# Performance work log

Hardware: AMD Instinct MI355X
Metric: run time of the kernel (lower is better)

Reference implementation:

```python
import jax, jax.numpy as jnp
import numpy as np

N_NODES = 50000
N_EDGES = 800000
IN_CH = 128
OUT_CH = 64


def setup_inputs() -> dict:
    key = jax.random.key(0)
    ks = jax.random.split(key, 8)
    cat = IN_CH + OUT_CH
    scale = 1.0 / np.sqrt(cat)
    return {
        "x": jax.random.normal(ks[0], (N_NODES, IN_CH), dtype=jnp.float32),
        "edge_index": jax.random.randint(ks[1], (2, N_EDGES), 0, N_NODES, dtype=jnp.int64),
        "edge_weight": jax.random.uniform(ks[2], (N_EDGES,), dtype=jnp.float32),
        "hidden_state": jax.random.normal(ks[3], (N_NODES, OUT_CH), dtype=jnp.float32),
        "W_z": jax.random.normal(ks[4], (cat, OUT_CH), dtype=jnp.float32) * scale,
        "b_z": jnp.zeros((OUT_CH,), dtype=jnp.float32),
        "W_r": jax.random.normal(ks[5], (cat, OUT_CH), dtype=jnp.float32) * scale,
        "b_r": jnp.zeros((OUT_CH,), dtype=jnp.float32),
        "W_h": jax.random.normal(ks[6], (cat, OUT_CH), dtype=jnp.float32) * scale,
        "b_h": jnp.zeros((OUT_CH,), dtype=jnp.float32),
    }


def _gcn_norm(row, col, w, num_nodes):
    # PyG GCNConv normalization with self-loops (fill_value=1):
    # norm_e = deg[row]^-1/2 * w_e * deg[col]^-1/2 over loop-augmented edges
    loops = jnp.arange(num_nodes, dtype=row.dtype)
    row = jnp.concatenate([row, loops])
    col = jnp.concatenate([col, loops])
    w = jnp.concatenate([w, jnp.ones((num_nodes,), dtype=w.dtype)])
    deg = jax.ops.segment_sum(w, col, num_segments=num_nodes)
    dinv = jnp.where(deg > 0, jax.lax.rsqrt(deg), 0.0)
    norm = dinv[row] * w * dinv[col]
    return row, col, norm


def _gcn_conv(x_cat, W, b, row, col, norm, num_nodes):
    h = x_cat @ W                                   # (N, out)
    msg = h[row] * norm[:, None]                    # (E+N, out) gather + scale
    out = jax.ops.segment_sum(msg, col, num_segments=num_nodes)
    return out + b


def reference(x, edge_index, edge_weight, hidden_state,
              W_z, b_z, W_r, b_r, W_h, b_h):
    n = x.shape[0]
    row, col, norm = _gcn_norm(edge_index[0], edge_index[1], edge_weight, n)
    xh = jnp.concatenate([x, hidden_state], axis=1)
    z = jax.nn.sigmoid(_gcn_conv(xh, W_z, b_z, row, col, norm, n))
    r = jax.nn.sigmoid(_gcn_conv(xh, W_r, b_r, row, col, norm, n))
    xrh = jnp.concatenate([x, r * hidden_state], axis=1)
    h_cand = jnp.tanh(_gcn_conv(xrh, W_h, b_h, row, col, norm, n))
    return z * hidden_state + (1.0 - z) * h_cand
```

## Files before the change

kernel.cpp:

```cpp
#include <hip/hip_runtime.h>
#include <hip/hip_bf16.h>
#include <cstdint>
#include <cstddef>

#define IN_CH   128
#define OUT_CH  64
#define CAT_CH  192

typedef short bf16x8 __attribute__((ext_vector_type(8)));
typedef float f32x4  __attribute__((ext_vector_type(4)));
typedef float f32x2  __attribute__((ext_vector_type(2)));
typedef unsigned long long u64;
typedef unsigned int u32;

__device__ __forceinline__ float sigmoidf_(float x) { return 1.f / (1.f + __expf(-x)); }

__device__ __forceinline__ unsigned short f2bf(float f) {
    u32 u = __float_as_uint(f);
    u32 r = (u + 0x7fffu + ((u >> 16) & 1u)) >> 16;
    return (unsigned short)r;
}
__device__ __forceinline__ u32 pk2bf(float a, float b) {
    return (u32)f2bf(a) | ((u32)f2bf(b) << 16);
}
__device__ __forceinline__ float bflo(u32 v) { return __uint_as_float(v << 16); }
__device__ __forceinline__ float bfhi(u32 v) { return __uint_as_float(v & 0xffff0000u); }

__device__ __forceinline__ unsigned char f2e4m3(float f) {
    u32 p = __builtin_amdgcn_cvt_pk_fp8_f32(f, f, 0, false);
    return (unsigned char)p;
}
template <bool HI>
__device__ __forceinline__ f32x2 fp8pk(u32 v) {
    return __builtin_amdgcn_cvt_pk_f32_fp8((int)v, HI);
}

__device__ __forceinline__ int load_col(const void* ei, int i, int E, int f) {
    return f ? ((const int*)ei)[E + i] : (int)((const long long*)ei)[E + i];
}
__device__ __forceinline__ int load_row(const void* ei, int i, int E, int f) {
    return f ? ((const int*)ei)[i] : (int)((const long long*)ei)[i];
}

__global__ void prep_kernel(int4* __restrict__ zdst, int n16,
                            const unsigned int* __restrict__ ei, int* __restrict__ flag,
                            const float* __restrict__ Wz, const float* __restrict__ Wr,
                            const float* __restrict__ Wh,
                            unsigned short* __restrict__ Bzrt, unsigned short* __restrict__ Wht,
                            int gZ) {
    int b = blockIdx.x, t = threadIdx.x;
    if (b < gZ) {
        int i = b * 256 + t;
        if (i < n16) zdst[i] = make_int4(0, 0, 0, 0);
    } else if (b == gZ) {
        if (t < 64) {
            unsigned int v = ei[(t << 1) + 1];
            unsigned long long bl = __ballot(v != 0u);
            if (t == 0) *flag = (bl != 0ull) ? 1 : 0;
        }
    } else {
        int i = (b - gZ - 1) * 256 + t;
        if (i < 192 * CAT_CH) {
            int col = i / CAT_CH, k = i % CAT_CH;
            if (col < 128) {
                float v = (col < 64) ? Wz[k * 64 + col] : Wr[k * 64 + (col - 64)];
                Bzrt[col * CAT_CH + k] = f2bf(v);
            } else {
                Wht[(col - 128) * CAT_CH + k] = f2bf(Wh[k * 64 + (col - 128)]);
            }
        }
    }
}

template <int TN, int OUT, bool A1F32>
__device__ __forceinline__ void gemm_body(
    unsigned short* __restrict__ As , unsigned short* __restrict__ Bs ,
    int blk, const float* __restrict__ A0, int a0w,
    const void* __restrict__ A1, int a1w,
    const unsigned short* __restrict__ Bt, int bOff, int K,
    const float* __restrict__ Cacc, void* __restrict__ Cout, int nrows)
{
    const int t = threadIdx.x, lane = t & 63, wave = t >> 6;
    const int rowBase = blk * 128;

    for (int idx = t * 8; idx < TN * K; idx += 256 * 8) {
        int col = idx / K, k = idx % K;
        *(int4*)&Bs[col * 200 + k] = *(const int4*)&Bt[col * CAT_CH + bOff + k];
    }

    f32x4 acc[2][TN / 16];
#pragma unroll
    for (int rf = 0; rf < 2; rf++)
#pragma unroll
        for (int cf = 0; cf < TN / 16; cf++) acc[rf][cf] = (f32x4){0.f, 0.f, 0.f, 0.f};

    const int srow = t >> 1, half = t & 1;
    int arow = rowBase + srow;
    if (arow >= nrows) arow = nrows - 1;

    for (int k0 = 0; k0 < K; k0 += 32) {
        __syncthreads();
        {
            int kk = k0 + half * 16;
            u32 pk[8];
            if (kk < a0w) {
                const float* src = A0 + (size_t)arow * a0w + kk;
#pragma unroll
                for (int q = 0; q < 4; q++) {
                    float4 v = *(const float4*)(src + q * 4);
                    pk[q * 2]     = pk2bf(v.x, v.y);
                    pk[q * 2 + 1] = pk2bf(v.z, v.w);
                }
            } else if (A1F32) {
                const float* src = (const float*)A1 + (size_t)arow * a1w + (kk - a0w);
#pragma unroll
                for (int q = 0; q < 4; q++) {
                    float4 v = *(const float4*)(src + q * 4);
                    pk[q * 2]     = pk2bf(v.x, v.y);
                    pk[q * 2 + 1] = pk2bf(v.z, v.w);
                }
            } else {
                const unsigned short* src =
                    (const unsigned short*)A1 + (size_t)arow * a1w + (kk - a0w);
                int4 v0 = *(const int4*)src;
                int4 v1 = *(const int4*)(src + 8);
                pk[0] = v0.x; pk[1] = v0.y; pk[2] = v0.z; pk[3] = v0.w;
                pk[4] = v1.x; pk[5] = v1.y; pk[6] = v1.z; pk[7] = v1.w;
            }
            *(int4*)&As[srow * 48 + half * 16]     = make_int4(pk[0], pk[1], pk[2], pk[3]);
            *(int4*)&As[srow * 48 + half * 16 + 8] = make_int4(pk[4], pk[5], pk[6], pk[7]);
        }
        __syncthreads();

        const int rbase = wave * 32;
        const int koff = (lane >> 4) * 8;
        bf16x8 a0 = *(const bf16x8*)&As[(rbase + (lane & 15)) * 48 + koff];
        bf16x8 a1 = *(const bf16x8*)&As[(rbase + 16 + (lane & 15)) * 48 + koff];
#pragma unroll
        for (int cf = 0; cf < TN / 16; cf++) {
            bf16x8 b = *(const bf16x8*)&Bs[(cf * 16 + (lane & 15)) * 200 + k0 + koff];
            acc[0][cf] = __builtin_amdgcn_mfma_f32_16x16x32_bf16(a0, b, acc[0][cf], 0, 0, 0);
            acc[1][cf] = __builtin_amdgcn_mfma_f32_16x16x32_bf16(a1, b, acc[1][cf], 0, 0, 0);
        }
    }

#pragma unroll
    for (int rf = 0; rf < 2; rf++)
#pragma unroll
        for (int cf = 0; cf < TN / 16; cf++) {
            int row0 = rowBase + wave * 32 + rf * 16 + (lane >> 4) * 4;
            int col  = cf * 16 + (lane & 15);
#pragma unroll
            for (int r = 0; r < 4; r++) {
                int row = row0 + r;
                if (row < nrows) {
                    float v = acc[rf][cf][r];
                    if (Cacc) v += Cacc[(size_t)row * TN + col];
                    if (OUT == 1)
                        ((unsigned char*)Cout)[(size_t)row * TN + col] = f2e4m3(v);
                    else if (OUT == 2)
                        ((float*)Cout)[(size_t)row * TN + col] = v;
                    else
                        ((unsigned short*)Cout)[(size_t)row * TN + col] = f2bf(v);
                }
            }
        }
}

__global__ __launch_bounds__(256) void work1_kernel(
    const float* __restrict__ x, const float* __restrict__ hidden,
    const unsigned short* __restrict__ Bzrt, const unsigned short* __restrict__ Wht,
    unsigned char* __restrict__ Hzr8, float* __restrict__ Hh32,
    const void* __restrict__ ei, const float* __restrict__ ew,
    u64* __restrict__ packed8, u32* __restrict__ rank,
    const int* __restrict__ flag, int E, int N, int gM)
{
    __shared__ unsigned short As[128 * 48];
    __shared__ unsigned short Bs[128 * 200];

    const int blk = blockIdx.x;
    int role, idx;
    if (blk < 3 * gM) { role = blk % 3; idx = blk / 3; }
    else              { role = 2;       idx = gM + (blk - 3 * gM); }

    if (role == 0) {
        gemm_body<128, 1, true>(As, Bs, idx, x, 128, (const void*)hidden, 64,
                                Bzrt, 0, 192, nullptr, (void*)Hzr8, N);
    } else if (role == 1) {
        gemm_body<64, 2, false>(As, Bs, idx, x, 128, nullptr, 0,
                                Wht, 0, 128, nullptr, (void*)Hh32, N);
    } else {
        int i0 = (idx * 256 + threadIdx.x) * 2;
        if (i0 >= E) return;
        const u32 shard = (u32)blk & 7;
        u64* __restrict__ shp = packed8 + (size_t)shard * N;
        int f = *flag;
        u32 rk[2];
#pragma unroll
        for (int k = 0; k < 2; k++) {
            int i = i0 + k;
            if (i < E) {
                int c = load_col(ei, i, E, f);
                u32 wq = __float2uint_rn(ew[i] * 1048576.0f);
                u64 old = atomicAdd(&shp[c], (1ull << 32) | (u64)wq);
                rk[k] = (shard << 28) | (u32)(old >> 32);
            }
        }
#pragma unroll
        for (int k = 0; k < 2; k++)
            if (i0 + k < E) rank[i0 + k] = rk[k];
    }
}

__global__ __launch_bounds__(256) void gemm2b_kernel(
    const unsigned short* __restrict__ RHb, const unsigned short* __restrict__ Wht,
    const float* __restrict__ Hh32, unsigned short* __restrict__ Hhb, int N)
{
    __shared__ unsigned short As[128 * 48];
    __shared__ unsigned short Bs[64 * 200];
    gemm_body<64, 0, false>(As, Bs, blockIdx.x, nullptr, 0, (const void*)RHb, 64,
                            Wht, 128, 64, Hh32, (void*)Hhb, N);
}

__global__ __launch_bounds__(256) void scan1_kernel(const u64* __restrict__ packed8,
                                                    float* __restrict__ dinv,
                                                    u32* __restrict__ shoff,
                                                    int* __restrict__ starts,
                                                    int* __restrict__ bsum, int n) {
    __shared__ int s[256];
    int i = blockIdx.x * 256 + threadIdx.x;
    int v = 0;
    if (i < n) {
        u32 run = 0, wsum = 0;
#pragma unroll
        for (int sh = 0; sh < 8; sh++) {
            u64 p = packed8[(size_t)sh * n + i];
            shoff[(size_t)sh * n + i] = run;
            run  += (u32)(p >> 32);
            wsum += (u32)p;
        }
        float ws = (float)wsum * (1.0f / 1048576.0f);
        dinv[i] = rsqrtf(1.0f + ws);
        v = (int)run;
    }
    s[threadIdx.x] = v;
    __syncthreads();
#pragma unroll
    for (int d = 1; d < 256; d <<= 1) {
        int t = (threadIdx.x >= d) ? s[threadIdx.x - d] : 0;
        __syncthreads();
        s[threadIdx.x] += t;
        __syncthreads();
    }
    if (i < n) starts[i] = s[threadIdx.x] - v;
    if (threadIdx.x == 255) bsum[blockIdx.x] = s[255];
}

__global__ __launch_bounds__(256) void scan2_kernel(int* __restrict__ bsum, int nb) {
    __shared__ int s[256];
    int t = threadIdx.x;
    int v = (t < nb) ? bsum[t] : 0;
    s[t] = v;
    __syncthreads();
#pragma unroll
    for (int d = 1; d < 256; d <<= 1) {
        int u = (t >= d) ? s[t - d] : 0;
        __syncthreads();
        s[t] += u;
        __syncthreads();
    }
    if (t < nb) bsum[t] = s[t] - v;
}

__global__ void scan3_kernel(int* __restrict__ starts, const int* __restrict__ boff,
                             int n, int E) {
    int i = blockIdx.x * blockDim.x + threadIdx.x;
    if (i == 0) starts[n] = E;
    if (i < n) starts[i] += boff[blockIdx.x];
}

__global__ void scatter2_kernel(const void* __restrict__ ei, const float* __restrict__ w,
                                const float* __restrict__ dinv, const int* __restrict__ starts,
                                const u32* __restrict__ shoff, const u32* __restrict__ rank,
                                u64* __restrict__ pairs, const int* __restrict__ flag,
                                int E, int N) {
    int i0 = (blockIdx.x * blockDim.x + threadIdx.x) * 4;
    if (i0 >= E) return;
    int f = *flag;
    int r[4], c[4];
#pragma unroll
    for (int k = 0; k < 4; k++) {
        int i = i0 + k;
        if (i < E) { r[k] = load_row(ei, i, E, f); c[k] = load_col(ei, i, E, f); }
    }
#pragma unroll
    for (int k = 0; k < 4; k++) {
        int i = i0 + k;
        if (i < E) {
            float nm = dinv[r[k]] * w[i] * dinv[c[k]];
            u32 rk = rank[i];
            u32 sh = rk >> 28, rks = rk & 0x0fffffffu;
            int pos = starts[c[k]] + (int)shoff[(size_t)sh * N + c[k]] + (int)rks;
            pairs[pos] = ((u64)__float_as_uint(nm) << 32) | (u32)(r[k] << 7);
        }
    }
}

__global__ __launch_bounds__(256) void spmm_zr_kernel(
    const unsigned char* __restrict__ H8, const u64* __restrict__ pairs,
    const int* __restrict__ starts, const float* __restrict__ dinv,
    const float* __restrict__ hidden, const float* __restrict__ bz,
    const float* __restrict__ br, float* __restrict__ Z,
    unsigned short* __restrict__ RHb, int N)
{
    int node = (blockIdx.x * 256 + threadIdx.x) >> 6;
    if (node >= N) return;
    const int lane = threadIdx.x & 63;
    const int sub = lane & 31, half = lane >> 5;
    int s = starts[node], e = starts[node + 1];
    float d = dinv[node], d2 = d * d;

    float a0 = 0.f, a1 = 0.f, a2 = 0.f, a3 = 0.f;
    if (half == 0) {
        u32 sv = *(const u32*)&H8[(size_t)node * 128 + sub * 4];
        f32x2 s01 = fp8pk<false>(sv), s23 = fp8pk<true>(sv);
        a0 = s01.x * d2; a1 = s01.y * d2; a2 = s23.x * d2; a3 = s23.y * d2;
    }

    int j = s;
    int full = s + ((e - s) & ~15);
    for (; j < full; j += 16) {
        u32 hv[8]; float nm[8];
#pragma unroll
        for (int k = 0; k < 8; k++) {
            u64 p = pairs[j + k * 2 + half];
            nm[k] = __uint_as_float((u32)(p >> 32));
            hv[k] = *(const u32*)&H8[(size_t)(u32)p + sub * 4];
        }
#pragma unroll
        for (int k = 0; k < 8; k++) {
            f32x2 h01 = fp8pk<false>(hv[k]), h23 = fp8pk<true>(hv[k]);
            a0 = fmaf(h01.x, nm[k], a0); a1 = fmaf(h01.y, nm[k], a1);
            a2 = fmaf(h23.x, nm[k], a2); a3 = fmaf(h23.y, nm[k], a3);
        }
    }
    if (j < e) {
        u32 hv[8]; float nm[8];
#pragma unroll
        for (int k = 0; k < 8; k++) {
            int jj = j + k * 2 + half;
            u64 p = pairs[(jj < e) ? jj : (e - 1)];
            nm[k] = (jj < e) ? __uint_as_float((u32)(p >> 32)) : 0.f;
            hv[k] = *(const u32*)&H8[(size_t)(u32)p + sub * 4];
        }
#pragma unroll
        for (int k = 0; k < 8; k++) {
            f32x2 h01 = fp8pk<false>(hv[k]), h23 = fp8pk<true>(hv[k]);
            a0 = fmaf(h01.x, nm[k], a0); a1 = fmaf(h01.y, nm[k], a1);
            a2 = fmaf(h23.x, nm[k], a2); a3 = fmaf(h23.y, nm[k], a3);
        }
    }

    a0 += __shfl_xor(a0, 32, 64);
    a1 += __shfl_xor(a1, 32, 64);
    a2 += __shfl_xor(a2, 32, 64);
    a3 += __shfl_xor(a3, 32, 64);

    if (half == 0) {
        if (sub < 16) {
            int c = sub * 4;
            float4 b4 = *(const float4*)&bz[c];
            float4 o = { sigmoidf_(a0 + b4.x), sigmoidf_(a1 + b4.y),
                         sigmoidf_(a2 + b4.z), sigmoidf_(a3 + b4.w) };
            *(float4*)&Z[(size_t)node * 64 + c] = o;
        } else {
            int c = (sub - 16) * 4;
            float4 b4 = *(const float4*)&br[c];
            float4 hid = *(const float4*)&hidden[(size_t)node * 64 + c];
            float r0 = sigmoidf_(a0 + b4.x) * hid.x;
            float r1 = sigmoidf_(a1 + b4.y) * hid.y;
            float r2 = sigmoidf_(a2 + b4.z) * hid.z;
            float r3 = sigmoidf_(a3 + b4.w) * hid.w;
            ushort4 o = { f2bf(r0), f2bf(r1), f2bf(r2), f2bf(r3) };
            *(ushort4*)&RHb[(size_t)node * 64 + c] = o;
        }
    }
}

__global__ __launch_bounds__(256) void spmm_h_kernel(
    const unsigned short* __restrict__ H, const u64* __restrict__ pairs,
    const int* __restrict__ starts, const float* __restrict__ dinv,
    const float* __restrict__ hidden, const float* __restrict__ bh,
    const float* __restrict__ Z, float* __restrict__ out, int N)
{
    int node = (blockIdx.x * 256 + threadIdx.x) >> 6;
    if (node >= N) return;
    const int lane = threadIdx.x & 63;
    const int sub = lane & 31, half = lane >> 5;
    const unsigned char* Hb = (const unsigned char*)H;
    int s = starts[node], e = starts[node + 1];
    float d = dinv[node], d2 = d * d;

    float ax = 0.f, ay = 0.f;
    if (half == 0) {
        u32 sv = *(const u32*)&Hb[(size_t)node * 128 + sub * 4];
        ax = bflo(sv) * d2; ay = bfhi(sv) * d2;
    }

    int j = s;
    int full = s + ((e - s) & ~15);
    for (; j < full; j += 16) {
        u32 hv[8]; float nm[8];
#pragma unroll
        for (int k = 0; k < 8; k++) {
            u64 p = pairs[j + k * 2 + half];
            nm[k] = __uint_as_float((u32)(p >> 32));
            hv[k] = *(const u32*)&Hb[(size_t)(u32)p + sub * 4];
        }
#pragma unroll
        for (int k = 0; k < 8; k++) {
            ax = fmaf(bflo(hv[k]), nm[k], ax);
            ay = fmaf(bfhi(hv[k]), nm[k], ay);
        }
    }
    if (j < e) {
        u32 hv[8]; float nm[8];
#pragma unroll
        for (int k = 0; k < 8; k++) {
            int jj = j + k * 2 + half;
            u64 p = pairs[(jj < e) ? jj : (e - 1)];
            nm[k] = (jj < e) ? __uint_as_float((u32)(p >> 32)) : 0.f;
            hv[k] = *(const u32*)&Hb[(size_t)(u32)p + sub * 4];
        }
#pragma unroll
        for (int k = 0; k < 8; k++) {
            ax = fmaf(bflo(hv[k]), nm[k], ax);
            ay = fmaf(bfhi(hv[k]), nm[k], ay);
        }
    }

    ax += __shfl_xor(ax, 32, 64);
    ay += __shfl_xor(ay, 32, 64);

    if (half == 0) {
        int c = sub * 2;
        size_t idx = (size_t)node * 64 + c;
        float2 hid = *(const float2*)&hidden[idx];
        float2 z   = *(const float2*)&Z[idx];
        float hc0 = tanhf(ax + bh[c]);
        float hc1 = tanhf(ay + bh[c + 1]);
        float2 o = { z.x * hid.x + (1.f - z.x) * hc0,
                     z.y * hid.y + (1.f - z.y) * hc1 };
        *(float2*)&out[idx] = o;
    }
}

extern "C" void kernel_launch(void* const* d_in, const int* in_sizes, int n_in,
                              void* d_out, int out_size, void* d_ws, size_t ws_size,
                              hipStream_t stream) {
    const float* x      = (const float*)d_in[0];
    const void*  eidx   = d_in[1];
    const float* ew     = (const float*)d_in[2];
    const float* hidden = (const float*)d_in[3];
    const float* Wz     = (const float*)d_in[4];
    const float* bz     = (const float*)d_in[5];
    const float* Wr     = (const float*)d_in[6];
    const float* br     = (const float*)d_in[7];
    const float* Wh     = (const float*)d_in[8];
    const float* bh     = (const float*)d_in[9];
    float* out = (float*)d_out;

    const int E = in_sizes[2];
    const int N = in_sizes[3] / OUT_CH;

    char* base = (char*)d_ws;
    size_t off = 0;
    auto carve = [&](size_t bytes) -> char* {
        char* p = base + off;
        off = (off + bytes + 255) & ~(size_t)255;
        return p;
    };
    u64*   packed8 = (u64*) carve((size_t)N * 8 * 8);
    u32*   shoff   = (u32*) carve((size_t)N * 8 * 4);
    u32*   rank    = (u32*) carve((size_t)E * 4);
    float* dinv    = (float*)carve((size_t)N * 4);
    int*   starts  = (int*)  carve((size_t)(N + 1) * 4);
    int*   bsum    = (int*)  carve(256 * 4);
    u64*   pairs   = (u64*)  carve((size_t)E * 8);
    unsigned char*  Hzr8 = (unsigned char*)carve((size_t)N * 128);
    unsigned short* RHb  = (unsigned short*)carve((size_t)N * 64 * 2);
    unsigned short* Hhb  = (unsigned short*)carve((size_t)N * 64 * 2);
    float* Hh32 = (float*)carve((size_t)N * 64 * 4);
    float* Z    = (float*)carve((size_t)N * 64 * 4);
    unsigned short* Bzrt = (unsigned short*)carve((size_t)128 * CAT_CH * 2);
    unsigned short* Wht  = (unsigned short*)carve((size_t)64 * CAT_CH * 2);
    int* flag = (int*)carve(4);
    if (off > ws_size) return;

    const int B256 = 256;
    const int gE2 = (E + 511) / 512;
    const int gE4 = (E + 1023) / 1024;
    const int gN = (N + B256 - 1) / B256;
    const int gM = (N + 127) / 128;
    const int gW = (N + 3) / 4;
    const int n16 = N * 4;
    const int gZ = (n16 + B256 - 1) / B256;
    const int gP = (192 * CAT_CH + 255) / 256;

    hipLaunchKernelGGL(prep_kernel, dim3(gZ + 1 + gP), dim3(B256), 0, stream,
                       (int4*)packed8, n16, (const unsigned int*)eidx, flag,
                       Wz, Wr, Wh, Bzrt, Wht, gZ);

    hipLaunchKernelGGL(work1_kernel, dim3(2 * gM + gE2), dim3(B256), 0, stream,
                       x, hidden, Bzrt, Wht, Hzr8, Hh32,
                       eidx, ew, packed8, rank, flag, E, N, gM);

    hipLaunchKernelGGL(scan1_kernel, dim3(gN), dim3(B256), 0, stream,
                       packed8, dinv, shoff, starts, bsum, N);
    hipLaunchKernelGGL(scan2_kernel, dim3(1), dim3(B256), 0, stream, bsum, gN);
    hipLaunchKernelGGL(scan3_kernel, dim3(gN), dim3(B256), 0, stream, starts, bsum, N, E);

    hipLaunchKernelGGL(scatter2_kernel, dim3(gE4), dim3(B256), 0, stream,
                       eidx, ew, dinv, starts, shoff, rank, pairs, flag, E, N);

    hipLaunchKernelGGL(spmm_zr_kernel, dim3(gW), dim3(B256), 0, stream,
                       Hzr8, pairs, starts, dinv, hidden, bz, br, Z, RHb, N);

    hipLaunchKernelGGL(gemm2b_kernel, dim3(gM), dim3(B256), 0, stream,
                       RHb, Wht, Hh32, Hhb, N);

    hipLaunchKernelGGL(spmm_h_kernel, dim3(gW), dim3(B256), 0, stream,
                       Hhb, pairs, starts, dinv, hidden, bh, Z, out, N);
}
```

Baseline: 165.5 us.

## Read GEMM B fragments directly from global memory and pad A tile stride

The B (weight) tile is no longer staged into shared memory. Each MFMA iteration instead loads its B fragment straight from global memory, which should mostly hit in L2/L1 because the weights are small. This cuts shared memory per block (the B tile was up to 51KB), which should raise occupancy in work1_kernel and gemm2b_kernel. The A tile row stride changes from 48 to 56 to reduce LDS bank conflicts. The cost is repeated global loads of B on every k-step, with latency that LDS would have hidden.

```diff
diff --git a/kernel.cpp b/kernel.cpp
--- a/kernel.cpp
+++ b/kernel.cpp
@@ -6,6 +6,7 @@
 #define IN_CH   128
 #define OUT_CH  64
 #define CAT_CH  192
+#define ALD     56
 
 typedef short bf16x8 __attribute__((ext_vector_type(8)));
 typedef float f32x4  __attribute__((ext_vector_type(4)));
@@ -74,7 +75,7 @@
 
 template <int TN, int OUT, bool A1F32>
 __device__ __forceinline__ void gemm_body(
-    unsigned short* __restrict__ As , unsigned short* __restrict__ Bs ,
+    unsigned short* __restrict__ As ,
     int blk, const float* __restrict__ A0, int a0w,
     const void* __restrict__ A1, int a1w,
     const unsigned short* __restrict__ Bt, int bOff, int K,
@@ -82,11 +83,6 @@
 {
     const int t = threadIdx.x, lane = t & 63, wave = t >> 6;
     const int rowBase = blk * 128;
-
-    for (int idx = t * 8; idx < TN * K; idx += 256 * 8) {
-        int col = idx / K, k = idx % K;
-        *(int4*)&Bs[col * 200 + k] = *(const int4*)&Bt[col * CAT_CH + bOff + k];
-    }
 
     f32x4 acc[2][TN / 16];
 #pragma unroll
@@ -127,18 +123,19 @@
                 pk[0] = v0.x; pk[1] = v0.y; pk[2] = v0.z; pk[3] = v0.w;
                 pk[4] = v1.x; pk[5] = v1.y; pk[6] = v1.z; pk[7] = v1.w;
             }
-            *(int4*)&As[srow * 48 + half * 16]     = make_int4(pk[0], pk[1], pk[2], pk[3]);
-            *(int4*)&As[srow * 48 + half * 16 + 8] = make_int4(pk[4], pk[5], pk[6], pk[7]);
+            *(int4*)&As[srow * ALD + half * 16]     = make_int4(pk[0], pk[1], pk[2], pk[3]);
+            *(int4*)&As[srow * ALD + half * 16 + 8] = make_int4(pk[4], pk[5], pk[6], pk[7]);
         }
         __syncthreads();
 
         const int rbase = wave * 32;
         const int koff = (lane >> 4) * 8;
-        bf16x8 a0 = *(const bf16x8*)&As[(rbase + (lane & 15)) * 48 + koff];
-        bf16x8 a1 = *(const bf16x8*)&As[(rbase + 16 + (lane & 15)) * 48 + koff];
+        bf16x8 a0 = *(const bf16x8*)&As[(rbase + (lane & 15)) * ALD + koff];
+        bf16x8 a1 = *(const bf16x8*)&As[(rbase + 16 + (lane & 15)) * ALD + koff];
 #pragma unroll
         for (int cf = 0; cf < TN / 16; cf++) {
-            bf16x8 b = *(const bf16x8*)&Bs[(cf * 16 + (lane & 15)) * 200 + k0 + koff];
+            bf16x8 b = *(const bf16x8*)
+                &Bt[(size_t)(cf * 16 + (lane & 15)) * CAT_CH + bOff + k0 + koff];
             acc[0][cf] = __builtin_amdgcn_mfma_f32_16x16x32_bf16(a0, b, acc[0][cf], 0, 0, 0);
             acc[1][cf] = __builtin_amdgcn_mfma_f32_16x16x32_bf16(a1, b, acc[1][cf], 0, 0, 0);
         }
@@ -175,8 +172,7 @@
     u64* __restrict__ packed8, u32* __restrict__ rank,
     const int* __restrict__ flag, int E, int N, int gM)
 {
-    __shared__ unsigned short As[128 * 48];
-    __shared__ unsigned short Bs[128 * 200];
+    __shared__ unsigned short As[128 * ALD];
 
     const int blk = blockIdx.x;
     int role, idx;
@@ -184,10 +180,10 @@
     else              { role = 2;       idx = gM + (blk - 3 * gM); }
 
     if (role == 0) {
-        gemm_body<128, 1, true>(As, Bs, idx, x, 128, (const void*)hidden, 64,
+        gemm_body<128, 1, true>(As, idx, x, 128, (const void*)hidden, 64,
                                 Bzrt, 0, 192, nullptr, (void*)Hzr8, N);
     } else if (role == 1) {
-        gemm_body<64, 2, false>(As, Bs, idx, x, 128, nullptr, 0,
+        gemm_body<64, 2, false>(As, idx, x, 128, nullptr, 0,
                                 Wht, 0, 128, nullptr, (void*)Hh32, N);
     } else {
         int i0 = (idx * 256 + threadIdx.x) * 2;
@@ -216,9 +212,8 @@
     const unsigned short* __restrict__ RHb, const unsigned short* __restrict__ Wht,
     const float* __restrict__ Hh32, unsigned short* __restrict__ Hhb, int N)
 {
-    __shared__ unsigned short As[128 * 48];
-    __shared__ unsigned short Bs[64 * 200];
-    gemm_body<64, 0, false>(As, Bs, blockIdx.x, nullptr, 0, (const void*)RHb, 64,
+    __shared__ unsigned short As[128 * ALD];
+    gemm_body<64, 0, false>(As, blockIdx.x, nullptr, 0, (const void*)RHb, 64,
                             Wht, 128, 64, Hh32, (void*)Hhb, N);
 }
 
```

After: 170.9 us. +3.3%, slower.
